# Optimization experiments

Measured on AMD Instinct MI355X. Metric: run time of the kernel, lower is better.

The kernel has to match this reference:

```python
import jax, jax.numpy as jnp
import numpy as np

D = 1024
K = 256
B = 8192


def setup_inputs() -> dict:
    key = jax.random.key(0)
    kx, kw, kd, kp = jax.random.split(key, 4)
    x = jax.random.normal(kx, (B, D), dtype=jnp.float32)
    # scale weights ~1/sqrt(d) so the 11-matmul chain stays numerically sane
    Ws = jax.random.normal(kw, (10, D, D), dtype=jnp.float32) / jnp.sqrt(jnp.float32(D))
    W_dec = jax.random.normal(kd, (D, K), dtype=jnp.float32) / jnp.sqrt(jnp.float32(K))
    perm = jax.random.randint(kp, (K,), 0, D, dtype=jnp.int64)
    return {"x": x, "Ws": Ws, "W_dec": W_dec, "perm": perm}


def reference(x, Ws, W_dec, perm):
    # torch nn.Linear(d,d,bias=False): y = x @ W.T
    # source applies fc1..fc9, then fc9 AGAIN, then fc10 (11 matmuls, 10 weights)
    order = list(range(9)) + [8, 9]
    h = x
    for i in order:
        h = h @ Ws[i].T  # [B, D]
    y = h[:, perm]        # vectorized gather, replaces per-row python loop [B, K]
    out = y @ W_dec.T     # fc_decode: [B, D]
    return out
```

## Files before the change

### kernel.cpp

```cpp
#include <hip/hip_runtime.h>
#include <stdint.h>
#include <stddef.h>

typedef __bf16 bf16;
typedef __bf16 bf16x8 __attribute__((ext_vector_type(8)));
typedef float f32x4 __attribute__((ext_vector_type(4)));

__device__ __forceinline__ void global_to_lds16(const void* g, void* l) {
  const __attribute__((address_space(1))) unsigned* gp =
      reinterpret_cast<const __attribute__((address_space(1))) unsigned*>(
          reinterpret_cast<uintptr_t>(g));
  __attribute__((address_space(3))) unsigned* lp =
      reinterpret_cast<__attribute__((address_space(3))) unsigned*>(
          reinterpret_cast<uintptr_t>(l));
  __builtin_amdgcn_global_load_lds(gp, lp, 16, 0, 0);
}

__device__ __forceinline__ void tile8x8_swizzle(int t, int& bx, int& by) {
  bx = (((t >> 3) & 1) << 2) | (t & 3);
  by = (((t >> 4) & 3) << 1) | ((t >> 2) & 1);
}

template <typename OutT>
__device__ __forceinline__ void gemm128_body(const bf16* __restrict__ A,
                                             const bf16* __restrict__ B,
                                             OutT* __restrict__ C,
                                             int bx, int by) {
  __shared__ bf16 As[2][128 * 64];
  __shared__ bf16 Bs[2][128 * 64];

  const int tid = threadIdx.x;
  const int wave = tid >> 6, lane = tid & 63;
  const int quad = lane >> 4, l16 = lane & 15;
  const int rowBase = by * 128;
  const int colBase = bx * 128;
  const int waveM = (wave >> 1) * 64, waveN = (wave & 1) * 64;

  const int sr = tid >> 2;
  const int sc = (tid & 3) * 8;
  const bf16* Ag0 = A + (size_t)(rowBase + sr) * 1024 + sc;
  const bf16* Ag1 = Ag0 + (size_t)64 * 1024;
  const bf16* Bg0 = B + (size_t)(colBase + sr) * 1024 + sc;
  const bf16* Bg1 = Bg0 + (size_t)64 * 1024;

  const int woff = wave * 1024;

  auto issue = [&](int k0, int p) {
    char* aB = (char*)As[p] + woff;
    char* bB = (char*)Bs[p] + woff;
    global_to_lds16(Ag0 + k0,      aB);
    global_to_lds16(Ag1 + k0,      aB + 4096);
    global_to_lds16(Ag0 + k0 + 32, aB + 8192);
    global_to_lds16(Ag1 + k0 + 32, aB + 12288);
    global_to_lds16(Bg0 + k0,      bB);
    global_to_lds16(Bg1 + k0,      bB + 4096);
    global_to_lds16(Bg0 + k0 + 32, bB + 8192);
    global_to_lds16(Bg1 + k0 + 32, bB + 12288);
  };

  f32x4 acc[4][4] = {};

  issue(0, 0);
  int p = 0;
#pragma unroll 1
  for (int k0 = 0; k0 < 1024; k0 += 64, p ^= 1) {
    __syncthreads();
    if (k0 + 64 < 1024) issue(k0 + 64, p ^ 1);
#pragma unroll
    for (int kk = 0; kk < 2; kk++) {
      const bf16* base = As[p] + kk * 4096;
      const bf16* baseB = Bs[p] + kk * 4096;
      bf16x8 af[4], bfr[4];
#pragma unroll
      for (int mi = 0; mi < 4; mi++)
        af[mi] = *(const bf16x8*)(base + (waveM + mi * 16 + l16) * 32 + quad * 8);
#pragma unroll
      for (int ni = 0; ni < 4; ni++)
        bfr[ni] = *(const bf16x8*)(baseB + (waveN + ni * 16 + l16) * 32 + quad * 8);
#pragma unroll
      for (int mi = 0; mi < 4; mi++)
#pragma unroll
        for (int ni = 0; ni < 4; ni++)
          acc[mi][ni] = __builtin_amdgcn_mfma_f32_16x16x32_bf16(af[mi], bfr[ni],
                                                                acc[mi][ni], 0, 0, 0);
    }
  }

  OutT* Cb = C + (size_t)(rowBase + waveM) * 1024 + colBase + waveN;
#pragma unroll
  for (int mi = 0; mi < 4; mi++)
#pragma unroll
    for (int ni = 0; ni < 4; ni++)
#pragma unroll
      for (int r = 0; r < 4; r++)
        Cb[(size_t)(mi * 16 + quad * 4 + r) * 1024 + ni * 16 + l16] =
            (OutT)acc[mi][ni][r];
}

template <typename OutT>
__device__ __forceinline__ void gemm128x64_body(const bf16* __restrict__ A,
                                                const bf16* __restrict__ B,
                                                OutT* __restrict__ C,
                                                int bx, int by) {
  __shared__ bf16 As[2][128 * 64];
  __shared__ bf16 Bs[2][64 * 64];

  const int tid = threadIdx.x;
  const int wave = tid >> 6, lane = tid & 63;
  const int quad = lane >> 4, l16 = lane & 15;
  const int rowBase = by * 128;
  const int colBase = bx * 64;
  const int waveM = (wave >> 1) * 64;
  const int waveN = (wave & 1) * 32;

  const int sr = tid >> 2;
  const int sc = (tid & 3) * 8;
  const bf16* Ag0 = A + (size_t)(rowBase + sr) * 1024 + sc;
  const bf16* Ag1 = Ag0 + (size_t)64 * 1024;
  const bf16* Bg0 = B + (size_t)(colBase + sr) * 1024 + sc;

  const int woff = wave * 1024;

  auto issue = [&](int k0, int p) {
    char* aB = (char*)As[p] + woff;
    char* bB = (char*)Bs[p] + woff;
    global_to_lds16(Ag0 + k0,      aB);
    global_to_lds16(Ag1 + k0,      aB + 4096);
    global_to_lds16(Ag0 + k0 + 32, aB + 8192);
    global_to_lds16(Ag1 + k0 + 32, aB + 12288);
    global_to_lds16(Bg0 + k0,      bB);
    global_to_lds16(Bg0 + k0 + 32, bB + 4096);
  };

  f32x4 acc[4][2] = {};

  issue(0, 0);
  int p = 0;
#pragma unroll 1
  for (int k0 = 0; k0 < 1024; k0 += 64, p ^= 1) {
    __syncthreads();
    if (k0 + 64 < 1024) issue(k0 + 64, p ^ 1);
#pragma unroll
    for (int kk = 0; kk < 2; kk++) {
      const bf16* base = As[p] + kk * 4096;
      const bf16* baseB = Bs[p] + kk * 2048;
      bf16x8 af[4], bfr[2];
#pragma unroll
      for (int mi = 0; mi < 4; mi++)
        af[mi] = *(const bf16x8*)(base + (waveM + mi * 16 + l16) * 32 + quad * 8);
#pragma unroll
      for (int ni = 0; ni < 2; ni++)
        bfr[ni] = *(const bf16x8*)(baseB + (waveN + ni * 16 + l16) * 32 + quad * 8);
#pragma unroll
      for (int mi = 0; mi < 4; mi++)
#pragma unroll
        for (int ni = 0; ni < 2; ni++)
          acc[mi][ni] = __builtin_amdgcn_mfma_f32_16x16x32_bf16(af[mi], bfr[ni],
                                                                acc[mi][ni], 0, 0, 0);
    }
  }

  OutT* Cb = C + (size_t)(rowBase + waveM) * 1024 + colBase + waveN;
#pragma unroll
  for (int mi = 0; mi < 4; mi++)
#pragma unroll
    for (int ni = 0; ni < 2; ni++)
#pragma unroll
      for (int r = 0; r < 4; r++)
        Cb[(size_t)(mi * 16 + quad * 4 + r) * 1024 + ni * 16 + l16] =
            (OutT)acc[mi][ni][r];
}

template <typename OutT>
__device__ __forceinline__ void gemm256x128_pipe(const bf16* __restrict__ A,
                                                 const bf16* __restrict__ B,
                                                 OutT* __restrict__ C,
                                                 int bx, int by) {
  __shared__ bf16 As[4][256 * 32];
  __shared__ bf16 Bs[4][128 * 32];

  const int tid = threadIdx.x;
  const int wave = tid >> 6, lane = tid & 63;
  const int quad = lane >> 4, l16 = lane & 15;
  const int rowBase = by * 256;
  const int colBase = bx * 128;
  const int waveM = (wave >> 1) * 64;
  const int waveN = (wave & 1) * 64;

  const int sr = tid >> 2;
  const int sg = ((tid & 3) ^ ((tid >> 3) & 3)) << 3;
  const bf16* Ag = A + (size_t)(rowBase + sr) * 1024 + sg;
  const bf16* Bg = B + (size_t)(colBase + sr) * 1024 + sg;
  const int woff = wave * 1024;

  auto issue = [&](int t) {
    const int k0 = t * 32;
    char* aB = (char*)As[t & 3] + woff;
    char* bB = (char*)Bs[t & 3] + woff;
    global_to_lds16(Ag + k0, aB);
    global_to_lds16(Ag + k0 + (size_t)128 * 1024, aB + 8192);
    global_to_lds16(Bg + k0, bB);
  };

  f32x4 acc[4][4] = {};

  issue(0); issue(1); issue(2);

  const int swz = (l16 >> 1) & 3;
#pragma unroll 1
  for (int i = 0; i < 32; ++i) {
    if (i <= 29)      asm volatile("s_waitcnt vmcnt(6)" ::: "memory");
    else if (i == 30) asm volatile("s_waitcnt vmcnt(3)" ::: "memory");
    else              asm volatile("s_waitcnt vmcnt(0)" ::: "memory");
    __builtin_amdgcn_s_barrier();
    __builtin_amdgcn_sched_barrier(0);
    if (i + 3 < 32) issue(i + 3);

    const bf16* bA = As[i & 3];
    const bf16* bB = Bs[i & 3];
    bf16x8 af[4], bfr[4];
#pragma unroll
    for (int mi = 0; mi < 4; mi++) {
      const int row = waveM + mi * 16 + l16;
      af[mi] = *(const bf16x8*)(bA + row * 32 + ((quad ^ swz) << 3));
    }
#pragma unroll
    for (int ni = 0; ni < 4; ni++) {
      const int row = waveN + ni * 16 + l16;
      bfr[ni] = *(const bf16x8*)(bB + row * 32 + ((quad ^ swz) << 3));
    }
#pragma unroll
    for (int mi = 0; mi < 4; mi++)
#pragma unroll
      for (int ni = 0; ni < 4; ni++)
        acc[mi][ni] = __builtin_amdgcn_mfma_f32_16x16x32_bf16(af[mi], bfr[ni],
                                                              acc[mi][ni], 0, 0, 0);
  }

  OutT* Cb = C + (size_t)(rowBase + waveM) * 1024 + colBase + waveN;
#pragma unroll
  for (int mi = 0; mi < 4; mi++)
#pragma unroll
    for (int ni = 0; ni < 4; ni++)
#pragma unroll
      for (int r = 0; r < 4; r++)
        Cb[(size_t)(mi * 16 + quad * 4 + r) * 1024 + ni * 16 + l16] =
            (OutT)acc[mi][ni][r];
}

struct PrepArgs {
  const float* cvt_src[5]; bf16* cvt_dst[5];
  const float* tr_src[6];  bf16* tr_dst[6];
  const float* Wdec; const int* praw; bf16* Gbf;
};

__global__ __launch_bounds__(256) void prep_all(PrepArgs p) {
  __shared__ alignas(16) char smem[64 * 65 * 2];
  const int b = blockIdx.x;
  const int tid = threadIdx.x;

  if (b < 2560) {
    const int m = b >> 9, blk = b & 511;
    const float* __restrict__ src = p.cvt_src[m];
    bf16* __restrict__ dst = p.cvt_dst[m];
    const int i = (blk * 256 + tid) * 8;
    float4 a = *(const float4*)(src + i);
    float4 c = *(const float4*)(src + i + 4);
    bf16x8 o;
    o[0] = (bf16)a.x; o[1] = (bf16)a.y; o[2] = (bf16)a.z; o[3] = (bf16)a.w;
    o[4] = (bf16)c.x; o[5] = (bf16)c.y; o[6] = (bf16)c.z; o[7] = (bf16)c.w;
    *(bf16x8*)(dst + i) = o;
  } else if (b < 4096) {
    const int t = b - 2560;
    const int m = t >> 8, r = t & 255;
    const float* __restrict__ src = p.tr_src[m];
    bf16* __restrict__ dst = p.tr_dst[m];
    bf16(*tile)[65] = reinterpret_cast<bf16(*)[65]>(smem);
    const int bx = (r & 15) * 64;
    const int by = (r >> 4) * 64;
    const int tx = tid & 63;
    const int ty4 = tid >> 6;
#pragma unroll
    for (int rr = 0; rr < 16; rr++) {
      int row = ty4 * 16 + rr;
      tile[row][tx] = (bf16)src[(size_t)(by + row) * 1024 + bx + tx];
    }
    __syncthreads();
#pragma unroll
    for (int rr = 0; rr < 16; rr++) {
      int row = ty4 * 16 + rr;
      dst[(size_t)(bx + row) * 1024 + by + tx] = tile[tx][row];
    }
  } else {
    const int j = b - 4096;
    float* row = (float*)smem;
    int* perm_l = (int*)(smem + 4096);
    int* nzp = (int*)(smem + 4096 + 1024);
#pragma unroll
    for (int c = 0; c < 4; c++) row[tid * 4 + c] = 0.f;
    if (tid == 0) *nzp = 0;
    __syncthreads();
    if (tid < 128 && p.praw[2 * tid + 1] != 0) atomicOr(nzp, 1);
    __syncthreads();
    const int is64 = (*nzp == 0);
    perm_l[tid] = is64 ? p.praw[2 * tid] : p.praw[tid];
    __syncthreads();
    atomicAdd(&row[perm_l[tid]], p.Wdec[(size_t)j * 256 + tid]);
    __syncthreads();
#pragma unroll
    for (int c = 0; c < 4; c++)
      p.Gbf[(size_t)j * 1024 + tid * 4 + c] = (bf16)row[tid * 4 + c];
  }
}

struct TreeArgs {
  const bf16* A[6]; const bf16* B[6]; bf16* C[6];
  int nG;
  const float* x; bf16* xbf; int ubase;
};

__global__ __launch_bounds__(256) void tree_level(TreeArgs a) {
  const int b = blockIdx.x;
  const int gBlocks = a.nG * 64;
  if (b < gBlocks) {
    const int z = b >> 6, t = b & 63;
    int bx, by;
    tile8x8_swizzle(t, bx, by);
    gemm128_body<bf16>(a.A[z], a.B[z], a.C[z], bx, by);
  } else {
    const int u0 = a.ubase + (b - gBlocks) * 8;
#pragma unroll
    for (int u = 0; u < 8; u++) {
      const int i = (u0 + u) * 2048 + (int)threadIdx.x * 8;
      float4 v0 = *(const float4*)(a.x + i);
      float4 v1 = *(const float4*)(a.x + i + 4);
      bf16x8 o;
      o[0] = (bf16)v0.x; o[1] = (bf16)v0.y; o[2] = (bf16)v0.z; o[3] = (bf16)v0.w;
      o[4] = (bf16)v1.x; o[5] = (bf16)v1.y; o[6] = (bf16)v1.z; o[7] = (bf16)v1.w;
      *(bf16x8*)(a.xbf + i) = o;
    }
  }
}

__global__ __launch_bounds__(256) void tree_level_hn(TreeArgs a) {
  const int b = blockIdx.x;
  if (b < 128) {
    gemm128x64_body<bf16>(a.A[0], a.B[0], a.C[0], b >> 3, b & 7);
  } else {
    const int u0 = a.ubase + (b - 128) * 8;
#pragma unroll
    for (int u = 0; u < 8; u++) {
      const int i = (u0 + u) * 2048 + (int)threadIdx.x * 8;
      float4 v0 = *(const float4*)(a.x + i);
      float4 v1 = *(const float4*)(a.x + i + 4);
      bf16x8 o;
      o[0] = (bf16)v0.x; o[1] = (bf16)v0.y; o[2] = (bf16)v0.z; o[3] = (bf16)v0.w;
      o[4] = (bf16)v1.x; o[5] = (bf16)v1.y; o[6] = (bf16)v1.z; o[7] = (bf16)v1.w;
      *(bf16x8*)(a.xbf + i) = o;
    }
  }
}

__global__ __launch_bounds__(512) void final_gemm(const bf16* __restrict__ A,
                                                  const bf16* __restrict__ B,
                                                  float* __restrict__ C) {
  const int b = blockIdx.x;
  const int j = b >> 3;
  const int by = (b & 7) * 4 + (j & 3);
  const int bx = j >> 2;
  gemm256x128_pipe<float>(A, B, C, bx, by);
}

extern "C" void kernel_launch(void* const* d_in, const int* in_sizes, int n_in,
                              void* d_out, int out_size, void* d_ws, size_t ws_size,
                              hipStream_t stream) {
  const float* x    = (const float*)d_in[0];
  const float* Wsrc = (const float*)d_in[1];
  const float* Wdec = (const float*)d_in[2];
  const int*   praw = (const int*)d_in[3];
  float* out = (float*)d_out;

  constexpr size_t MAT  = 1024ull * 1024ull;
  constexpr size_t SLOT = 2ull * 1024 * 1024;

  char* ws = (char*)d_ws;
  bf16* Wrm[5];
  for (int i = 0; i < 5; i++) Wrm[i] = (bf16*)(ws + (size_t)i * SLOT);
  bf16* Wt[6];
  for (int i = 0; i < 6; i++) Wt[i] = (bf16*)(ws + (size_t)(5 + i) * SLOT);
  bf16* Gbf = (bf16*)(ws + 11 * SLOT);
  bf16* xbf = (bf16*)(ws + 12 * SLOT);
  bf16* P[6];
  for (int i = 0; i < 6; i++) P[i] = (bf16*)(ws + (size_t)(20 + i) * SLOT);
  bf16* Q[3];
  for (int i = 0; i < 3; i++) Q[i] = (bf16*)(ws + (size_t)(26 + i) * SLOT);
  bf16* Rb = (bf16*)(ws + 29 * SLOT);
  bf16* Fb = (bf16*)(ws + 30 * SLOT);

  PrepArgs pa;
  const int rmIdx[5] = {1, 3, 5, 7, 8};
  for (int i = 0; i < 5; i++) { pa.cvt_src[i] = Wsrc + (size_t)rmIdx[i] * MAT; pa.cvt_dst[i] = Wrm[i]; }
  const int trIdx[6] = {0, 2, 4, 6, 8, 9};
  for (int i = 0; i < 6; i++) { pa.tr_src[i] = Wsrc + (size_t)trIdx[i] * MAT; pa.tr_dst[i] = Wt[i]; }
  pa.Wdec = Wdec; pa.praw = praw; pa.Gbf = Gbf;
  prep_all<<<dim3(5120), 256, 0, stream>>>(pa);

  TreeArgs L1{};
  const bf16* l1a[6] = {Gbf, Wt[4], Wrm[3], Wt[2], Wrm[1], Wt[0]};
  const bf16* l1b[6] = {Wt[5], Wrm[4], Wt[3], Wrm[2], Wt[1], Wrm[0]};
  for (int i = 0; i < 6; i++) { L1.A[i] = l1a[i]; L1.B[i] = l1b[i]; L1.C[i] = P[i]; }
  L1.nG = 6; L1.x = x; L1.xbf = xbf; L1.ubase = 0;
  tree_level<<<dim3(384 + 256), 256, 0, stream>>>(L1);

  TreeArgs L2{};
  const bf16* l2a[3] = {P[0], P[3], P[5]};
  const bf16* l2b[3] = {P[1], P[2], P[4]};
  for (int i = 0; i < 3; i++) { L2.A[i] = l2a[i]; L2.B[i] = l2b[i]; L2.C[i] = Q[i]; }
  L2.nG = 3; L2.x = x; L2.xbf = xbf; L2.ubase = 2048;
  tree_level<<<dim3(192 + 128), 256, 0, stream>>>(L2);

  TreeArgs L3{};
  L3.A[0] = Q[0]; L3.B[0] = Q[1]; L3.C[0] = Rb;
  L3.nG = 1; L3.x = x; L3.xbf = xbf; L3.ubase = 3072;
  tree_level_hn<<<dim3(128 + 64), 256, 0, stream>>>(L3);

  TreeArgs L4{};
  L4.A[0] = Rb; L4.B[0] = Q[2]; L4.C[0] = Fb;
  L4.nG = 1; L4.x = x; L4.xbf = xbf; L4.ubase = 3584;
  tree_level_hn<<<dim3(128 + 64), 256, 0, stream>>>(L4);

  final_gemm<<<dim3(256), 512, 0, stream>>>(xbf, Fb, out);

  (void)in_sizes; (void)n_in; (void)out_size; (void)ws_size;
}
```

Measured before the change: 196.1 us.

## Split final GEMM over K with atomic float accumulation and fused zeroing

The final 8192x1024x1024 GEMM is now split into two K halves, doubling the block count from 256 to 512 so more CUs are occupied. Each block adds its partial result into the output with float atomicAdd. The output is zeroed by extra blocks appended to the two preceding tree-level launches. The LDS pipeline is reduced from 4-stage with explicit vmcnt waits to simple double buffering with __syncthreads. The costs are atomic traffic on 8M output elements, extra zeroing writes, a shallower prefetch pipeline, and nondeterministic summation order.

```diff
diff --git a/kernel.cpp b/kernel.cpp
--- a/kernel.cpp
+++ b/kernel.cpp
@@ -171,13 +171,12 @@
             (OutT)acc[mi][ni][r];
 }
 
-template <typename OutT>
-__device__ __forceinline__ void gemm256x128_pipe(const bf16* __restrict__ A,
-                                                 const bf16* __restrict__ B,
-                                                 OutT* __restrict__ C,
-                                                 int bx, int by) {
-  __shared__ bf16 As[4][256 * 32];
-  __shared__ bf16 Bs[4][128 * 32];
+__device__ __forceinline__ void gemm256x128_splitk(const bf16* __restrict__ A,
+                                                   const bf16* __restrict__ B,
+                                                   float* __restrict__ C,
+                                                   int bx, int by, int kbeg) {
+  __shared__ bf16 As[2][256 * 32];
+  __shared__ bf16 Bs[2][128 * 32];
 
   const int tid = threadIdx.x;
   const int wave = tid >> 6, lane = tid & 63;
@@ -193,10 +192,9 @@
   const bf16* Bg = B + (size_t)(colBase + sr) * 1024 + sg;
   const int woff = wave * 1024;
 
-  auto issue = [&](int t) {
-    const int k0 = t * 32;
-    char* aB = (char*)As[t & 3] + woff;
-    char* bB = (char*)Bs[t & 3] + woff;
+  auto issue = [&](int k0, int p) {
+    char* aB = (char*)As[p] + woff;
+    char* bB = (char*)Bs[p] + woff;
     global_to_lds16(Ag + k0, aB);
     global_to_lds16(Ag + k0 + (size_t)128 * 1024, aB + 8192);
     global_to_lds16(Bg + k0, bB);
@@ -204,20 +202,15 @@
 
   f32x4 acc[4][4] = {};
 
-  issue(0); issue(1); issue(2);
-
+  issue(kbeg, 0);
+  int p = 0;
   const int swz = (l16 >> 1) & 3;
 #pragma unroll 1
-  for (int i = 0; i < 32; ++i) {
-    if (i <= 29)      asm volatile("s_waitcnt vmcnt(6)" ::: "memory");
-    else if (i == 30) asm volatile("s_waitcnt vmcnt(3)" ::: "memory");
-    else              asm volatile("s_waitcnt vmcnt(0)" ::: "memory");
-    __builtin_amdgcn_s_barrier();
-    __builtin_amdgcn_sched_barrier(0);
-    if (i + 3 < 32) issue(i + 3);
-
-    const bf16* bA = As[i & 3];
-    const bf16* bB = Bs[i & 3];
+  for (int i = 0; i < 16; ++i, p ^= 1) {
+    __syncthreads();
+    if (i + 1 < 16) issue(kbeg + (i + 1) * 32, p ^ 1);
+    const bf16* bA = As[p];
+    const bf16* bB = Bs[p];
     bf16x8 af[4], bfr[4];
 #pragma unroll
     for (int mi = 0; mi < 4; mi++) {
@@ -237,15 +230,15 @@
                                                               acc[mi][ni], 0, 0, 0);
   }
 
-  OutT* Cb = C + (size_t)(rowBase + waveM) * 1024 + colBase + waveN;
+  float* Cb = C + (size_t)(rowBase + waveM) * 1024 + colBase + waveN;
 #pragma unroll
   for (int mi = 0; mi < 4; mi++)
 #pragma unroll
     for (int ni = 0; ni < 4; ni++)
 #pragma unroll
       for (int r = 0; r < 4; r++)
-        Cb[(size_t)(mi * 16 + quad * 4 + r) * 1024 + ni * 16 + l16] =
-            (OutT)acc[mi][ni][r];
+        atomicAdd(&Cb[(size_t)(mi * 16 + quad * 4 + r) * 1024 + ni * 16 + l16],
+                  acc[mi][ni][r]);
 }
 
 struct PrepArgs {
@@ -317,6 +310,7 @@
   const bf16* A[6]; const bf16* B[6]; bf16* C[6];
   int nG;
   const float* x; bf16* xbf; int ubase;
+  float* zout; int zbase;
 };
 
 __global__ __launch_bounds__(256) void tree_level(TreeArgs a) {
@@ -346,7 +340,7 @@
   const int b = blockIdx.x;
   if (b < 128) {
     gemm128x64_body<bf16>(a.A[0], a.B[0], a.C[0], b >> 3, b & 7);
-  } else {
+  } else if (b < 192) {
     const int u0 = a.ubase + (b - 128) * 8;
 #pragma unroll
     for (int u = 0; u < 8; u++) {
@@ -358,6 +352,12 @@
       o[4] = (bf16)v1.x; o[5] = (bf16)v1.y; o[6] = (bf16)v1.z; o[7] = (bf16)v1.w;
       *(bf16x8*)(a.xbf + i) = o;
     }
+  } else {
+    float4* o4 = (float4*)(a.zout + (size_t)(a.zbase + (b - 192)) * 65536);
+    const float4 z4 = {0.f, 0.f, 0.f, 0.f};
+#pragma unroll
+    for (int u = 0; u < 64; u++)
+      o4[u * 256 + (int)threadIdx.x] = z4;
   }
 }
 
@@ -365,10 +365,12 @@
                                                   const bf16* __restrict__ B,
                                                   float* __restrict__ C) {
   const int b = blockIdx.x;
-  const int j = b >> 3;
-  const int by = (b & 7) * 4 + (j & 3);
+  const int t = b & 255;
+  const int kbeg = (b >> 8) * 512;
+  const int j = t >> 3;
+  const int by = (t & 7) * 4 + (j & 3);
   const int bx = j >> 2;
-  gemm256x128_pipe<float>(A, B, C, bx, by);
+  gemm256x128_splitk(A, B, C, bx, by, kbeg);
 }
 
 extern "C" void kernel_launch(void* const* d_in, const int* in_sizes, int n_in,
@@ -422,14 +424,16 @@
   TreeArgs L3{};
   L3.A[0] = Q[0]; L3.B[0] = Q[1]; L3.C[0] = Rb;
   L3.nG = 1; L3.x = x; L3.xbf = xbf; L3.ubase = 3072;
-  tree_level_hn<<<dim3(128 + 64), 256, 0, stream>>>(L3);
+  L3.zout = out; L3.zbase = 0;
+  tree_level_hn<<<dim3(256), 256, 0, stream>>>(L3);
 
   TreeArgs L4{};
   L4.A[0] = Rb; L4.B[0] = Q[2]; L4.C[0] = Fb;
   L4.nG = 1; L4.x = x; L4.xbf = xbf; L4.ubase = 3584;
-  tree_level_hn<<<dim3(128 + 64), 256, 0, stream>>>(L4);
-
-  final_gemm<<<dim3(256), 512, 0, stream>>>(xbf, Fb, out);
+  L4.zout = out; L4.zbase = 64;
+  tree_level_hn<<<dim3(256), 256, 0, stream>>>(L4);
+
+  final_gemm<<<dim3(512), 512, 0, stream>>>(xbf, Fb, out);
 
   (void)in_sizes; (void)n_in; (void)out_size; (void)ws_size;
 }
```

Measured after the change: 239.0 us. 1.22x slower.

## Split final GEMM K-step into two MFMA phases and rebalance tree-level work

Applied to the files above, without the earlier changes.

The final 256x128 GEMM main loop now runs in two halves per K-step. Each half loads its B fragments, passes a barrier, and issues MFMAs at raised wave priority (s_setprio), which is meant to interleave LDS reads, global prefetch issue and MFMA work across waves. Separately, level 2 of the weight-product tree switches to the 128x64-tile kernel (generalised to several GEMMs), giving 384 blocks instead of 192 for better CU occupancy. The x-to-bf16 conversion work is spread evenly across the four tree levels. The extra barriers per iteration add synchronisation cost, and the waitcnt shift must keep the prefetch ordering correct.

```diff
diff --git a/kernel.cpp b/kernel.cpp
--- a/kernel.cpp
+++ b/kernel.cpp
@@ -172,10 +172,10 @@
 }
 
 template <typename OutT>
-__device__ __forceinline__ void gemm256x128_pipe(const bf16* __restrict__ A,
-                                                 const bf16* __restrict__ B,
-                                                 OutT* __restrict__ C,
-                                                 int bx, int by) {
+__device__ __forceinline__ void gemm256x128_8ph(const bf16* __restrict__ A,
+                                                const bf16* __restrict__ B,
+                                                OutT* __restrict__ C,
+                                                int bx, int by) {
   __shared__ bf16 As[4][256 * 32];
   __shared__ bf16 Bs[4][128 * 32];
 
@@ -205,36 +205,50 @@
   f32x4 acc[4][4] = {};
 
   issue(0); issue(1); issue(2);
-
-  const int swz = (l16 >> 1) & 3;
+  asm volatile("s_waitcnt vmcnt(6)" ::: "memory");
+  asm volatile("s_barrier" ::: "memory");
+
+  const int gq = ((quad ^ ((l16 >> 1) & 3)) << 3);
 #pragma unroll 1
   for (int i = 0; i < 32; ++i) {
-    if (i <= 29)      asm volatile("s_waitcnt vmcnt(6)" ::: "memory");
-    else if (i == 30) asm volatile("s_waitcnt vmcnt(3)" ::: "memory");
-    else              asm volatile("s_waitcnt vmcnt(0)" ::: "memory");
-    __builtin_amdgcn_s_barrier();
-    __builtin_amdgcn_sched_barrier(0);
-    if (i + 3 < 32) issue(i + 3);
-
     const bf16* bA = As[i & 3];
     const bf16* bB = Bs[i & 3];
     bf16x8 af[4], bfr[4];
-#pragma unroll
-    for (int mi = 0; mi < 4; mi++) {
-      const int row = waveM + mi * 16 + l16;
-      af[mi] = *(const bf16x8*)(bA + row * 32 + ((quad ^ swz) << 3));
-    }
-#pragma unroll
-    for (int ni = 0; ni < 4; ni++) {
-      const int row = waveN + ni * 16 + l16;
-      bfr[ni] = *(const bf16x8*)(bB + row * 32 + ((quad ^ swz) << 3));
-    }
+
 #pragma unroll
     for (int mi = 0; mi < 4; mi++)
-#pragma unroll
-      for (int ni = 0; ni < 4; ni++)
+      af[mi] = *(const bf16x8*)(bA + (waveM + mi * 16 + l16) * 32 + gq);
+#pragma unroll
+    for (int ni = 0; ni < 2; ni++)
+      bfr[ni] = *(const bf16x8*)(bB + (waveN + ni * 16 + l16) * 32 + gq);
+    if (i + 3 < 32) issue(i + 3);
+    asm volatile("s_barrier" ::: "memory");
+    __builtin_amdgcn_s_setprio(1);
+#pragma unroll
+    for (int mi = 0; mi < 4; mi++)
+#pragma unroll
+      for (int ni = 0; ni < 2; ni++)
         acc[mi][ni] = __builtin_amdgcn_mfma_f32_16x16x32_bf16(af[mi], bfr[ni],
                                                               acc[mi][ni], 0, 0, 0);
+    __builtin_amdgcn_s_setprio(0);
+    asm volatile("s_barrier" ::: "memory");
+
+#pragma unroll
+    for (int ni = 2; ni < 4; ni++)
+      bfr[ni] = *(const bf16x8*)(bB + (waveN + ni * 16 + l16) * 32 + gq);
+    if (i <= 28)      asm volatile("s_waitcnt vmcnt(6)" ::: "memory");
+    else if (i == 29) asm volatile("s_waitcnt vmcnt(3)" ::: "memory");
+    else if (i == 30) asm volatile("s_waitcnt vmcnt(0)" ::: "memory");
+    asm volatile("s_barrier" ::: "memory");
+    __builtin_amdgcn_s_setprio(1);
+#pragma unroll
+    for (int mi = 0; mi < 4; mi++)
+#pragma unroll
+      for (int ni = 2; ni < 4; ni++)
+        acc[mi][ni] = __builtin_amdgcn_mfma_f32_16x16x32_bf16(af[mi], bfr[ni],
+                                                              acc[mi][ni], 0, 0, 0);
+    __builtin_amdgcn_s_setprio(0);
+    asm volatile("s_barrier" ::: "memory");
   }
 
   OutT* Cb = C + (size_t)(rowBase + waveM) * 1024 + colBase + waveN;
@@ -344,10 +358,12 @@
 
 __global__ __launch_bounds__(256) void tree_level_hn(TreeArgs a) {
   const int b = blockIdx.x;
-  if (b < 128) {
-    gemm128x64_body<bf16>(a.A[0], a.B[0], a.C[0], b >> 3, b & 7);
+  const int gBlocks = a.nG * 128;
+  if (b < gBlocks) {
+    const int z = b >> 7, t = b & 127;
+    gemm128x64_body<bf16>(a.A[z], a.B[z], a.C[z], t >> 3, t & 7);
   } else {
-    const int u0 = a.ubase + (b - 128) * 8;
+    const int u0 = a.ubase + (b - gBlocks) * 8;
 #pragma unroll
     for (int u = 0; u < 8; u++) {
       const int i = (u0 + u) * 2048 + (int)threadIdx.x * 8;
@@ -368,7 +384,7 @@
   const int j = b >> 3;
   const int by = (b & 7) * 4 + (j & 3);
   const int bx = j >> 2;
-  gemm256x128_pipe<float>(A, B, C, bx, by);
+  gemm256x128_8ph<float>(A, B, C, bx, by);
 }
 
 extern "C" void kernel_launch(void* const* d_in, const int* in_sizes, int n_in,
@@ -410,24 +426,24 @@
   const bf16* l1b[6] = {Wt[5], Wrm[4], Wt[3], Wrm[2], Wt[1], Wrm[0]};
   for (int i = 0; i < 6; i++) { L1.A[i] = l1a[i]; L1.B[i] = l1b[i]; L1.C[i] = P[i]; }
   L1.nG = 6; L1.x = x; L1.xbf = xbf; L1.ubase = 0;
-  tree_level<<<dim3(384 + 256), 256, 0, stream>>>(L1);
+  tree_level<<<dim3(384 + 128), 256, 0, stream>>>(L1);
 
   TreeArgs L2{};
   const bf16* l2a[3] = {P[0], P[3], P[5]};
   const bf16* l2b[3] = {P[1], P[2], P[4]};
   for (int i = 0; i < 3; i++) { L2.A[i] = l2a[i]; L2.B[i] = l2b[i]; L2.C[i] = Q[i]; }
-  L2.nG = 3; L2.x = x; L2.xbf = xbf; L2.ubase = 2048;
-  tree_level<<<dim3(192 + 128), 256, 0, stream>>>(L2);
+  L2.nG = 3; L2.x = x; L2.xbf = xbf; L2.ubase = 1024;
+  tree_level_hn<<<dim3(384 + 128), 256, 0, stream>>>(L2);
 
   TreeArgs L3{};
   L3.A[0] = Q[0]; L3.B[0] = Q[1]; L3.C[0] = Rb;
-  L3.nG = 1; L3.x = x; L3.xbf = xbf; L3.ubase = 3072;
-  tree_level_hn<<<dim3(128 + 64), 256, 0, stream>>>(L3);
+  L3.nG = 1; L3.x = x; L3.xbf = xbf; L3.ubase = 2048;
+  tree_level_hn<<<dim3(128 + 128), 256, 0, stream>>>(L3);
 
   TreeArgs L4{};
   L4.A[0] = Rb; L4.B[0] = Q[2]; L4.C[0] = Fb;
-  L4.nG = 1; L4.x = x; L4.xbf = xbf; L4.ubase = 3584;
-  tree_level_hn<<<dim3(128 + 64), 256, 0, stream>>>(L4);
+  L4.nG = 1; L4.x = x; L4.xbf = xbf; L4.ubase = 3072;
+  tree_level_hn<<<dim3(128 + 128), 256, 0, stream>>>(L4);
 
   final_gemm<<<dim3(256), 512, 0, stream>>>(xbf, Fb, out);
 
```

After: 195.1 us. About the same (-0.5%).
